# Kernel tuning notes

Measured on AMD Instinct MI355X. Metric: run time of the kernel, lower is better.

Reference implementation:

```python
import jax, jax.numpy as jnp
import numpy as np

D_MODEL = 768
N_HEADS = 12
D_HEAD = D_MODEL // N_HEADS


def setup_inputs() -> dict:
    key = jax.random.key(0)
    ks = jax.random.split(key, 6)
    B, T = 2, 4096
    x = jax.random.normal(ks[0], (B, T, D_MODEL), dtype=jnp.float32)
    mask = jnp.ones((B, T), dtype=jnp.int32)
    # torch nn.Linear: weight [out, in], bias [out]
    s_in = 1.0 / np.sqrt(D_MODEL)
    w_qkv = jax.random.uniform(ks[1], (3 * D_MODEL, D_MODEL), jnp.float32, -s_in, s_in)
    b_qkv = jax.random.uniform(ks[2], (3 * D_MODEL,), jnp.float32, -s_in, s_in)
    w_out = jax.random.uniform(ks[3], (D_MODEL, D_MODEL), jnp.float32, -s_in, s_in)
    b_out = jax.random.uniform(ks[4], (D_MODEL,), jnp.float32, -s_in, s_in)
    return {"x": x, "w_qkv": w_qkv, "b_qkv": b_qkv, "w_out": w_out, "b_out": b_out, "mask": mask}


def reference(x, w_qkv, b_qkv, w_out, b_out, mask):
    B, T, C = x.shape
    # fused QKV projection: [B,T,3C]
    qkv = x @ w_qkv.T + b_qkv
    qkv = qkv.reshape(B, T, 3, N_HEADS, D_HEAD)
    qkv = jnp.transpose(qkv, (2, 0, 3, 1, 4))  # [3,B,H,T,Dh]
    q, k, v = qkv[0], qkv[1], qkv[2]
    scale = jnp.float32(np.sqrt(D_HEAD))
    scores = jnp.einsum('bhqd,bhkd->bhqk', q, k) / scale  # [B,H,T,T]
    scores = jnp.where(mask[:, None, None, :] == 0, jnp.float32(-1e9), scores)
    weights = jax.nn.softmax(scores, axis=-1)  # dropout p=0 (eval-mode reference)
    out = jnp.einsum('bhqk,bhkd->bhqd', weights, v)  # [B,H,T,Dh]
    out = jnp.transpose(out, (0, 2, 1, 3)).reshape(B, T, C)
    return out @ w_out.T + b_out
```

## Files before the change

kernel.cpp:

```cpp
#include <hip/hip_runtime.h>
#include <hip/hip_bf16.h>
#include <cstdint>
#include <cstddef>

#define D_MODEL 768
#define N_HEADS 12
#define T_SEQ   4096
#define B_BATCH 2
#define BT      (B_BATCH * T_SEQ)

typedef __attribute__((ext_vector_type(8))) short bf16x8;
typedef __attribute__((ext_vector_type(4))) float f32x4;

__device__ __forceinline__ short fbf(float f) {
  __hip_bfloat16 h = __float2bfloat16(f);
  return __builtin_bit_cast(short, h);
}

__device__ __forceinline__ void gl_lds16(const void* g, void* l) {
  __builtin_amdgcn_global_load_lds(
      (const __attribute__((address_space(1))) void*)g,
      (__attribute__((address_space(3))) void*)l, 16, 0, 0);
}

__global__ __launch_bounds__(256) void cast_bf16(const float* __restrict__ in,
                                                 short* __restrict__ out, int n8) {
  int i = blockIdx.x * 256 + threadIdx.x;
  if (i >= n8) return;
  const float4* p = (const float4*)in + (size_t)i * 2;
  float4 v0 = p[0], v1 = p[1];
  bf16x8 o;
  o[0] = fbf(v0.x); o[1] = fbf(v0.y); o[2] = fbf(v0.z); o[3] = fbf(v0.w);
  o[4] = fbf(v1.x); o[5] = fbf(v1.y); o[6] = fbf(v1.z); o[7] = fbf(v1.w);
  *(bf16x8*)(out + (size_t)i * 8) = o;
}

__global__ __launch_bounds__(256) void mask_prep(const int* __restrict__ mask,
                                                 short* __restrict__ maskpb) {
  int t = blockIdx.x * 256 + threadIdx.x;
  int blk = t >> 6, j = t & 63;
  int pj = (((j >> 4) & 1) << 5) | (((j >> 2) & 3) << 3) | (((j >> 5) & 1) << 2) | (j & 3);
  maskpb[blk * 64 + pj] = mask[t] ? (short)0x3F80 : (short)0;
}

template<int EPI>
__global__ __launch_bounds__(256) void gemm_bt(
    const short* __restrict__ A, const short* __restrict__ Bm,
    const float* __restrict__ bias, int K, int N,
    short* __restrict__ Qb, short* __restrict__ Kb, short* __restrict__ Vt,
    const int* __restrict__ maskp, float* __restrict__ Cout)
{
  __shared__ __align__(16) short As[128 * 64];
  __shared__ __align__(16) short Bs[128 * 64];

  const int t = threadIdx.x;
  const int lane = t & 63, wave = t >> 6;
  const int a = lane & 15, g = lane >> 4;
  const int wr = wave >> 1, wc = wave & 1;
  const int bm = blockIdx.x * 128, bn = blockIdx.y * 128;

  f32x4 acc[4][4];
  #pragma unroll
  for (int i = 0; i < 4; ++i)
    #pragma unroll
    for (int j = 0; j < 4; ++j) acc[i][j] = f32x4{0.f, 0.f, 0.f, 0.f};

  const int nkt = K >> 6;
  for (int kt = 0; kt < nkt; ++kt) {
    const int k0 = kt << 6;
    __syncthreads();
    #pragma unroll
    for (int it = 0; it < 4; ++it) {
      int cid = it * 256 + t;
      int row = cid >> 3, c16 = cid & 7;
      int sc = c16 ^ (row & 7);
      gl_lds16(A  + (size_t)(bm + row) * K + k0 + sc * 8, (char*)As + (it * 256 + wave * 64) * 16);
      gl_lds16(Bm + (size_t)(bn + row) * K + k0 + sc * 8, (char*)Bs + (it * 256 + wave * 64) * 16);
    }
    __syncthreads();
    #pragma unroll
    for (int c = 0; c < 2; ++c) {
      bf16x8 af[4], bfr[4];
      #pragma unroll
      for (int mi = 0; mi < 4; ++mi) {
        int row = wr * 64 + mi * 16 + a;
        af[mi] = *(const bf16x8*)((const char*)As + row * 128 + ((c * 64 + g * 16) ^ ((row & 7) << 4)));
      }
      #pragma unroll
      for (int ni = 0; ni < 4; ++ni) {
        int row = wc * 64 + ni * 16 + a;
        bfr[ni] = *(const bf16x8*)((const char*)Bs + row * 128 + ((c * 64 + g * 16) ^ ((row & 7) << 4)));
      }
      #pragma unroll
      for (int mi = 0; mi < 4; ++mi)
        #pragma unroll
        for (int ni = 0; ni < 4; ++ni)
          acc[mi][ni] = __builtin_amdgcn_mfma_f32_16x16x32_bf16(af[mi], bfr[ni], acc[mi][ni], 0, 0, 0);
    }
  }

  if (EPI == 1) {
    #pragma unroll
    for (int mi = 0; mi < 4; ++mi) {
      int rowb = bm + wr * 64 + mi * 16 + g * 4;
      #pragma unroll
      for (int ni = 0; ni < 4; ++ni) {
        int col = bn + wc * 64 + ni * 16 + a;
        float bv = bias[col];
        #pragma unroll
        for (int r = 0; r < 4; ++r)
          Cout[(size_t)(rowb + r) * N + col] = acc[mi][ni][r] + bv;
      }
    }
  } else {
    const float QSCALE = 0.125f * 1.44269504088896f;
    const int sec = bn / D_MODEL;
    #pragma unroll
    for (int ni = 0; ni < 4; ++ni) {
      int n = bn + wc * 64 + ni * 16 + a;
      int wcol = n - sec * D_MODEL;
      int h = wcol >> 6, d = wcol & 63;
      float bv = bias[n];
      #pragma unroll
      for (int mi = 0; mi < 4; ++mi) {
        #pragma unroll
        for (int r = 0; r < 4; ++r) {
          int mrow = bm + wr * 64 + mi * 16 + g * 4 + r;
          int bb = mrow >> 12, tt = mrow & 4095;
          float val = acc[mi][ni][r] + bv;
          size_t bhoff = (size_t)(bb * N_HEADS + h);
          if (sec == 0)       Qb[(bhoff * T_SEQ + tt) * 64 + d] = fbf(val * QSCALE);
          else if (sec == 1)  Kb[(bhoff * T_SEQ + tt) * 64 + d] = fbf(val);
          else {
            val *= (float)maskp[(size_t)bb * T_SEQ + tt];
            int t6 = tt & 63;
            int ttp = (tt & ~63) | (((t6 >> 4) & 1) << 5) | (((t6 >> 2) & 3) << 3)
                    | (((t6 >> 5) & 1) << 2) | (t6 & 3);
            Vt[(bhoff * 64 + d) * T_SEQ + ttp] = fbf(val);
          }
        }
      }
    }
  }
}

__global__ __launch_bounds__(256, 3) void attn(
    const short* __restrict__ Qb, const short* __restrict__ Kb, const short* __restrict__ Vt,
    const short* __restrict__ maskpb, short* __restrict__ Ao)
{
  __shared__ __align__(16) short Kt[2][64 * 64];
  __shared__ __align__(16) short Vs[2][64 * 64];

  const int t = threadIdx.x;
  const int lane = t & 63, wave = t >> 6;
  const int a = lane & 15, g = lane >> 4;

  const int flat = blockIdx.x;
  const int xcd = flat & 7, slot = flat >> 3;
  const int logical = xcd * 96 + slot;
  const int bh = logical >> 5;
  const int qblk = logical & 31;

  const int b = bh / N_HEADS, h = bh - b * N_HEADS;
  const size_t headoff = (size_t)bh * T_SEQ * 64;
  const int q0 = qblk * 128 + wave * 32;

  const int srow0 = t >> 3, sc0 = (t & 7) ^ (srow0 & 7);
  const int srow1 = (256 + t) >> 3, sc1 = (t & 7) ^ (srow1 & 7);
  const short* Kh = Kb + headoff;
  const short* Vh = Vt + headoff;
  const short* mh = maskpb + (size_t)b * T_SEQ;

  bf16x8 qf[2][2];
  #pragma unroll
  for (int qg = 0; qg < 2; ++qg) {
    const short* qrow = Qb + headoff + (size_t)(q0 + qg * 16 + a) * 64;
    qf[qg][0] = *(const bf16x8*)(qrow + g * 8);
    qf[qg][1] = *(const bf16x8*)(qrow + 32 + g * 8);
  }

  int foff[2][4];
  #pragma unroll
  for (int c = 0; c < 2; ++c)
    #pragma unroll
    for (int ni = 0; ni < 4; ++ni) {
      int row = ni * 16 + a;
      foff[c][ni] = row * 128 + ((c * 64 + g * 16) ^ ((row & 7) << 4));
    }

  f32x4 o[2][4];
  f32x4 ladd[2];
  #pragma unroll
  for (int qg = 0; qg < 2; ++qg) {
    ladd[qg] = f32x4{0.f, 0.f, 0.f, 0.f};
    #pragma unroll
    for (int i = 0; i < 4; ++i) o[qg][i] = f32x4{0.f, 0.f, 0.f, 0.f};
  }

#define STAGE(buf, kb)                                                                   \
  do {                                                                                   \
    gl_lds16(Kh + (size_t)((kb) + srow0) * 64 + sc0 * 8, (char*)Kt[buf] + (wave * 64) * 16);          \
    gl_lds16(Vh + (size_t)srow0 * T_SEQ + (kb) + sc0 * 8, (char*)Vs[buf] + (wave * 64) * 16);         \
    gl_lds16(Kh + (size_t)((kb) + srow1) * 64 + sc1 * 8, (char*)Kt[buf] + (256 + wave * 64) * 16);    \
    gl_lds16(Vh + (size_t)srow1 * T_SEQ + (kb) + sc1 * 8, (char*)Vs[buf] + (256 + wave * 64) * 16);   \
  } while (0)

  STAGE(0, 0);
  __syncthreads();

  const int NT = T_SEQ / 64;
  int cur = 0;
  for (int kt = 0; kt < NT; ++kt) {
    const int kb = kt * 64;
    if (kt + 1 < NT) STAGE(cur ^ 1, kb + 64);

    f32x4 st[2][4];
    #pragma unroll
    for (int qg = 0; qg < 2; ++qg)
      #pragma unroll
      for (int ni = 0; ni < 4; ++ni) st[qg][ni] = f32x4{0.f,0.f,0.f,0.f};

    __builtin_amdgcn_s_setprio(1);
    #pragma unroll
    for (int c = 0; c < 2; ++c) {
      #pragma unroll
      for (int ni = 0; ni < 4; ++ni) {
        bf16x8 kf = *(const bf16x8*)((const char*)Kt[cur] + foff[c][ni]);
        st[0][ni] = __builtin_amdgcn_mfma_f32_16x16x32_bf16(kf, qf[0][c], st[0][ni], 0, 0, 0);
        st[1][ni] = __builtin_amdgcn_mfma_f32_16x16x32_bf16(kf, qf[1][c], st[1][ni], 0, 0, 0);
      }
    }
    __builtin_amdgcn_s_setprio(0);

    bf16x8 pa[2][2];
    #pragma unroll
    for (int qg = 0; qg < 2; ++qg)
      #pragma unroll
      for (int ni = 0; ni < 4; ++ni) {
        const int c = ni & 1, jb = (ni >> 1) * 4;
        #pragma unroll
        for (int r = 0; r < 4; ++r)
          pa[qg][c][jb + r] = fbf(__builtin_amdgcn_exp2f(st[qg][ni][r]));
      }

    __builtin_amdgcn_s_setprio(1);
    #pragma unroll
    for (int c = 0; c < 2; ++c) {
      bf16x8 mbf = *(const bf16x8*)(mh + kb + c * 32 + g * 8);
      ladd[0] = __builtin_amdgcn_mfma_f32_16x16x32_bf16(pa[0][c], mbf, ladd[0], 0, 0, 0);
      ladd[1] = __builtin_amdgcn_mfma_f32_16x16x32_bf16(pa[1][c], mbf, ladd[1], 0, 0, 0);
      #pragma unroll
      for (int di = 0; di < 4; ++di) {
        bf16x8 vf = *(const bf16x8*)((const char*)Vs[cur] + foff[c][di]);
        o[0][di] = __builtin_amdgcn_mfma_f32_16x16x32_bf16(pa[0][c], vf, o[0][di], 0, 0, 0);
        o[1][di] = __builtin_amdgcn_mfma_f32_16x16x32_bf16(pa[1][c], vf, o[1][di], 0, 0, 0);
      }
    }
    __builtin_amdgcn_s_setprio(0);

    __syncthreads();
    cur ^= 1;
  }
#undef STAGE

  #pragma unroll
  for (int qg = 0; qg < 2; ++qg) {
    float linv[4];
    #pragma unroll
    for (int r = 0; r < 4; ++r) linv[r] = 1.f / ladd[qg][r];
    #pragma unroll
    for (int di = 0; di < 4; ++di)
      #pragma unroll
      for (int r = 0; r < 4; ++r) {
        int rowg = b * T_SEQ + q0 + qg * 16 + g * 4 + r;
        Ao[(size_t)rowg * D_MODEL + h * 64 + di * 16 + a] = fbf(o[qg][di][r] * linv[r]);
      }
  }
}

extern "C" void kernel_launch(void* const* d_in, const int* in_sizes, int n_in,
                              void* d_out, int out_size, void* d_ws, size_t ws_size,
                              hipStream_t stream) {
  const float* x     = (const float*)d_in[0];
  const float* w_qkv = (const float*)d_in[1];
  const float* b_qkv = (const float*)d_in[2];
  const float* w_out = (const float*)d_in[3];
  const float* b_out = (const float*)d_in[4];
  const int*   mask  = (const int*)d_in[5];
  float* out = (float*)d_out;

  char* w = (char*)d_ws;
  short* xb     = (short*)w; w += (size_t)BT * D_MODEL * 2;
  short* wqkvb  = (short*)w; w += (size_t)3 * D_MODEL * D_MODEL * 2;
  short* woutb  = (short*)w; w += (size_t)D_MODEL * D_MODEL * 2;
  short* Qb     = (short*)w; w += (size_t)BT * D_MODEL * 2;
  short* Kb     = (short*)w; w += (size_t)BT * D_MODEL * 2;
  short* Vt     = (short*)w; w += (size_t)BT * D_MODEL * 2;
  short* Ao     = (short*)w; w += (size_t)BT * D_MODEL * 2;
  short* maskpb = (short*)w; w += (size_t)BT * 2;

  {
    int n8 = BT * D_MODEL / 8;
    cast_bf16<<<n8 / 256, 256, 0, stream>>>(x, xb, n8);
  }
  {
    int n8 = 3 * D_MODEL * D_MODEL / 8;
    cast_bf16<<<n8 / 256, 256, 0, stream>>>(w_qkv, wqkvb, n8);
  }
  {
    int n8 = D_MODEL * D_MODEL / 8;
    cast_bf16<<<n8 / 256, 256, 0, stream>>>(w_out, woutb, n8);
  }
  mask_prep<<<BT / 256, 256, 0, stream>>>(mask, maskpb);

  gemm_bt<0><<<dim3(BT / 128, 3 * D_MODEL / 128), 256, 0, stream>>>(
      xb, wqkvb, b_qkv, D_MODEL, 3 * D_MODEL, Qb, Kb, Vt, mask, nullptr);

  attn<<<768, 256, 0, stream>>>(Qb, Kb, Vt, maskpb, Ao);

  gemm_bt<1><<<dim3(BT / 128, D_MODEL / 128), 256, 0, stream>>>(
      Ao, woutb, b_out, D_MODEL, D_MODEL, nullptr, nullptr, nullptr, nullptr, out);
}
```

Before: 268.6 us.

## Triple-buffer attention K/V, fold mask into K/V, coalesce V-transpose stores

The attention loop moves from double to triple buffering of K/V tiles in LDS. It uses an explicit vmcnt wait and a single barrier per iteration, so loads for tile kt+2 overlap compute on tile kt. The per-tile mask load in the row-sum MFMA is removed: masked keys get K and V zeroed in the QKV epilogue, the row sum uses a constant ones vector, and the count of masked keys is subtracted from the denominator. The V epilogue now stages the transposed, permuted tile through LDS so global stores are coalesced. LDS use per block rises, and the denominator trick depends on masked scores being exactly zero.

```diff
diff --git a/kernel.cpp b/kernel.cpp
--- a/kernel.cpp
+++ b/kernel.cpp
@@ -35,12 +35,18 @@
   *(bf16x8*)(out + (size_t)i * 8) = o;
 }
 
-__global__ __launch_bounds__(256) void mask_prep(const int* __restrict__ mask,
-                                                 short* __restrict__ maskpb) {
-  int t = blockIdx.x * 256 + threadIdx.x;
-  int blk = t >> 6, j = t & 63;
-  int pj = (((j >> 4) & 1) << 5) | (((j >> 2) & 3) << 3) | (((j >> 5) & 1) << 2) | (j & 3);
-  maskpb[blk * 64 + pj] = mask[t] ? (short)0x3F80 : (short)0;
+__global__ __launch_bounds__(256) void mask_count(const int* __restrict__ mask,
+                                                  float* __restrict__ nm) {
+  __shared__ int red[256];
+  int s = 0;
+  for (int i = threadIdx.x; i < T_SEQ; i += 256) s += mask[blockIdx.x * T_SEQ + i];
+  red[threadIdx.x] = s;
+  __syncthreads();
+  for (int off = 128; off > 0; off >>= 1) {
+    if (threadIdx.x < off) red[threadIdx.x] += red[threadIdx.x + off];
+    __syncthreads();
+  }
+  if (threadIdx.x == 0) nm[blockIdx.x] = (float)(T_SEQ - red[0]);
 }
 
 template<int EPI>
@@ -50,8 +56,11 @@
     short* __restrict__ Qb, short* __restrict__ Kb, short* __restrict__ Vt,
     const int* __restrict__ maskp, float* __restrict__ Cout)
 {
-  __shared__ __align__(16) short As[128 * 64];
-  __shared__ __align__(16) short Bs[128 * 64];
+  __shared__ __align__(16) short smem[128 * 132];
+  short* As = smem;
+  short* Bs = smem + 128 * 64;
+  typedef short CtRow[132];
+  CtRow* Ct = (CtRow*)smem;
 
   const int t = threadIdx.x;
   const int lane = t & 63, wave = t >> 6;
@@ -115,41 +124,66 @@
   } else {
     const float QSCALE = 0.125f * 1.44269504088896f;
     const int sec = bn / D_MODEL;
-    #pragma unroll
-    for (int ni = 0; ni < 4; ++ni) {
-      int n = bn + wc * 64 + ni * 16 + a;
-      int wcol = n - sec * D_MODEL;
-      int h = wcol >> 6, d = wcol & 63;
-      float bv = bias[n];
-      #pragma unroll
-      for (int mi = 0; mi < 4; ++mi) {
-        #pragma unroll
-        for (int r = 0; r < 4; ++r) {
-          int mrow = bm + wr * 64 + mi * 16 + g * 4 + r;
-          int bb = mrow >> 12, tt = mrow & 4095;
-          float val = acc[mi][ni][r] + bv;
-          size_t bhoff = (size_t)(bb * N_HEADS + h);
-          if (sec == 0)       Qb[(bhoff * T_SEQ + tt) * 64 + d] = fbf(val * QSCALE);
-          else if (sec == 1)  Kb[(bhoff * T_SEQ + tt) * 64 + d] = fbf(val);
-          else {
-            val *= (float)maskp[(size_t)bb * T_SEQ + tt];
-            int t6 = tt & 63;
-            int ttp = (tt & ~63) | (((t6 >> 4) & 1) << 5) | (((t6 >> 2) & 3) << 3)
-                    | (((t6 >> 5) & 1) << 2) | (t6 & 3);
-            Vt[(bhoff * 64 + d) * T_SEQ + ttp] = fbf(val);
+    const int bb = bm >> 12, tt0 = bm & 4095;
+    if (sec < 2) {
+      #pragma unroll
+      for (int ni = 0; ni < 4; ++ni) {
+        int n = bn + wc * 64 + ni * 16 + a;
+        int wcol = n - sec * D_MODEL;
+        int h = wcol >> 6, d = wcol & 63;
+        float bv = bias[n];
+        size_t bhoff = (size_t)(bb * N_HEADS + h);
+        #pragma unroll
+        for (int mi = 0; mi < 4; ++mi) {
+          #pragma unroll
+          for (int r = 0; r < 4; ++r) {
+            int tt = tt0 + wr * 64 + mi * 16 + g * 4 + r;
+            float val = acc[mi][ni][r] + bv;
+            if (sec == 0) Qb[(bhoff * T_SEQ + tt) * 64 + d] = fbf(val * QSCALE);
+            else          Kb[(bhoff * T_SEQ + tt) * 64 + d] =
+                              fbf(val * (float)maskp[(size_t)bb * T_SEQ + tt]);
           }
         }
       }
+    } else {
+      __syncthreads();
+      #pragma unroll
+      for (int ni = 0; ni < 4; ++ni) {
+        int col_t = wc * 64 + ni * 16 + a;
+        float bv = bias[bn + col_t];
+        #pragma unroll
+        for (int mi = 0; mi < 4; ++mi) {
+          #pragma unroll
+          for (int r = 0; r < 4; ++r) {
+            int rowin = wr * 64 + mi * 16 + g * 4 + r;
+            int tt = tt0 + rowin;
+            float val = (acc[mi][ni][r] + bv) * (float)maskp[(size_t)bb * T_SEQ + tt];
+            int t6 = rowin & 63;
+            int rowp = (rowin & 64) | (((t6 >> 4) & 1) << 5) | (((t6 >> 2) & 3) << 3)
+                     | (((t6 >> 5) & 1) << 2) | (t6 & 3);
+            Ct[col_t][rowp] = fbf(val);
+          }
+        }
+      }
+      __syncthreads();
+      const int wb = bn - 2 * D_MODEL;
+      #pragma unroll
+      for (int it = 0; it < 32; ++it) {
+        int col = wave * 32 + it;
+        int wcol = wb + col;
+        int h = wcol >> 6, d = wcol & 63;
+        size_t base = ((size_t)(bb * N_HEADS + h) * 64 + d) * T_SEQ + tt0;
+        *(short2*)(Vt + base + 2 * lane) = *(const short2*)&Ct[col][2 * lane];
+      }
     }
   }
 }
 
 __global__ __launch_bounds__(256, 3) void attn(
     const short* __restrict__ Qb, const short* __restrict__ Kb, const short* __restrict__ Vt,
-    const short* __restrict__ maskpb, short* __restrict__ Ao)
+    const float* __restrict__ nmasked, short* __restrict__ Ao)
 {
-  __shared__ __align__(16) short Kt[2][64 * 64];
-  __shared__ __align__(16) short Vs[2][64 * 64];
+  __shared__ __align__(16) short KV[3][2][64 * 64];
 
   const int t = threadIdx.x;
   const int lane = t & 63, wave = t >> 6;
@@ -169,7 +203,7 @@
   const int srow1 = (256 + t) >> 3, sc1 = (t & 7) ^ (srow1 & 7);
   const short* Kh = Kb + headoff;
   const short* Vh = Vt + headoff;
-  const short* mh = maskpb + (size_t)b * T_SEQ;
+  const float nm = nmasked[b];
 
   bf16x8 qf[2][2];
   #pragma unroll
@@ -179,6 +213,10 @@
     qf[qg][1] = *(const bf16x8*)(qrow + 32 + g * 8);
   }
 
+  bf16x8 ones;
+  #pragma unroll
+  for (int i = 0; i < 8; ++i) ones[i] = (short)0x3F80;
+
   int foff[2][4];
   #pragma unroll
   for (int c = 0; c < 2; ++c)
@@ -197,22 +235,27 @@
     for (int i = 0; i < 4; ++i) o[qg][i] = f32x4{0.f, 0.f, 0.f, 0.f};
   }
 
-#define STAGE(buf, kb)                                                                   \
-  do {                                                                                   \
-    gl_lds16(Kh + (size_t)((kb) + srow0) * 64 + sc0 * 8, (char*)Kt[buf] + (wave * 64) * 16);          \
-    gl_lds16(Vh + (size_t)srow0 * T_SEQ + (kb) + sc0 * 8, (char*)Vs[buf] + (wave * 64) * 16);         \
-    gl_lds16(Kh + (size_t)((kb) + srow1) * 64 + sc1 * 8, (char*)Kt[buf] + (256 + wave * 64) * 16);    \
-    gl_lds16(Vh + (size_t)srow1 * T_SEQ + (kb) + sc1 * 8, (char*)Vs[buf] + (256 + wave * 64) * 16);   \
+#define STAGE(buf, kb)                                                                        \
+  do {                                                                                        \
+    gl_lds16(Kh + (size_t)((kb) + srow0) * 64 + sc0 * 8,  (char*)KV[buf][0] + (wave * 64) * 16);       \
+    gl_lds16(Vh + (size_t)srow0 * T_SEQ + (kb) + sc0 * 8, (char*)KV[buf][1] + (wave * 64) * 16);       \
+    gl_lds16(Kh + (size_t)((kb) + srow1) * 64 + sc1 * 8,  (char*)KV[buf][0] + (256 + wave * 64) * 16); \
+    gl_lds16(Vh + (size_t)srow1 * T_SEQ + (kb) + sc1 * 8, (char*)KV[buf][1] + (256 + wave * 64) * 16); \
   } while (0)
 
   STAGE(0, 0);
-  __syncthreads();
+  STAGE(1, 64);
 
   const int NT = T_SEQ / 64;
-  int cur = 0;
+  int cur = 0, nx2 = 2;
   for (int kt = 0; kt < NT; ++kt) {
-    const int kb = kt * 64;
-    if (kt + 1 < NT) STAGE(cur ^ 1, kb + 64);
+    if (kt < NT - 1) asm volatile("s_waitcnt vmcnt(4)" ::: "memory");
+    else             asm volatile("s_waitcnt vmcnt(0)" ::: "memory");
+    __builtin_amdgcn_s_barrier();
+    if (kt + 2 < NT) STAGE(nx2, (kt + 2) * 64);
+
+    const char* Ktc = (const char*)KV[cur][0];
+    const char* Vsc = (const char*)KV[cur][1];
 
     f32x4 st[2][4];
     #pragma unroll
@@ -225,7 +268,7 @@
     for (int c = 0; c < 2; ++c) {
       #pragma unroll
       for (int ni = 0; ni < 4; ++ni) {
-        bf16x8 kf = *(const bf16x8*)((const char*)Kt[cur] + foff[c][ni]);
+        bf16x8 kf = *(const bf16x8*)(Ktc + foff[c][ni]);
         st[0][ni] = __builtin_amdgcn_mfma_f32_16x16x32_bf16(kf, qf[0][c], st[0][ni], 0, 0, 0);
         st[1][ni] = __builtin_amdgcn_mfma_f32_16x16x32_bf16(kf, qf[1][c], st[1][ni], 0, 0, 0);
       }
@@ -246,20 +289,19 @@
     __builtin_amdgcn_s_setprio(1);
     #pragma unroll
     for (int c = 0; c < 2; ++c) {
-      bf16x8 mbf = *(const bf16x8*)(mh + kb + c * 32 + g * 8);
-      ladd[0] = __builtin_amdgcn_mfma_f32_16x16x32_bf16(pa[0][c], mbf, ladd[0], 0, 0, 0);
-      ladd[1] = __builtin_amdgcn_mfma_f32_16x16x32_bf16(pa[1][c], mbf, ladd[1], 0, 0, 0);
+      ladd[0] = __builtin_amdgcn_mfma_f32_16x16x32_bf16(pa[0][c], ones, ladd[0], 0, 0, 0);
+      ladd[1] = __builtin_amdgcn_mfma_f32_16x16x32_bf16(pa[1][c], ones, ladd[1], 0, 0, 0);
       #pragma unroll
       for (int di = 0; di < 4; ++di) {
-        bf16x8 vf = *(const bf16x8*)((const char*)Vs[cur] + foff[c][di]);
+        bf16x8 vf = *(const bf16x8*)(Vsc + foff[c][di]);
         o[0][di] = __builtin_amdgcn_mfma_f32_16x16x32_bf16(pa[0][c], vf, o[0][di], 0, 0, 0);
         o[1][di] = __builtin_amdgcn_mfma_f32_16x16x32_bf16(pa[1][c], vf, o[1][di], 0, 0, 0);
       }
     }
     __builtin_amdgcn_s_setprio(0);
 
-    __syncthreads();
-    cur ^= 1;
+    cur = cur + 1; if (cur == 3) cur = 0;
+    nx2 = nx2 + 1; if (nx2 == 3) nx2 = 0;
   }
 #undef STAGE
 
@@ -267,7 +309,7 @@
   for (int qg = 0; qg < 2; ++qg) {
     float linv[4];
     #pragma unroll
-    for (int r = 0; r < 4; ++r) linv[r] = 1.f / ladd[qg][r];
+    for (int r = 0; r < 4; ++r) linv[r] = 1.f / (ladd[qg][r] - nm);
     #pragma unroll
     for (int di = 0; di < 4; ++di)
       #pragma unroll
@@ -290,14 +332,14 @@
   float* out = (float*)d_out;
 
   char* w = (char*)d_ws;
-  short* xb     = (short*)w; w += (size_t)BT * D_MODEL * 2;
-  short* wqkvb  = (short*)w; w += (size_t)3 * D_MODEL * D_MODEL * 2;
-  short* woutb  = (short*)w; w += (size_t)D_MODEL * D_MODEL * 2;
-  short* Qb     = (short*)w; w += (size_t)BT * D_MODEL * 2;
-  short* Kb     = (short*)w; w += (size_t)BT * D_MODEL * 2;
-  short* Vt     = (short*)w; w += (size_t)BT * D_MODEL * 2;
-  short* Ao     = (short*)w; w += (size_t)BT * D_MODEL * 2;
-  short* maskpb = (short*)w; w += (size_t)BT * 2;
+  short* xb    = (short*)w; w += (size_t)BT * D_MODEL * 2;
+  short* wqkvb = (short*)w; w += (size_t)3 * D_MODEL * D_MODEL * 2;
+  short* woutb = (short*)w; w += (size_t)D_MODEL * D_MODEL * 2;
+  short* Qb    = (short*)w; w += (size_t)BT * D_MODEL * 2;
+  short* Kb    = (short*)w; w += (size_t)BT * D_MODEL * 2;
+  short* Vt    = (short*)w; w += (size_t)BT * D_MODEL * 2;
+  short* Ao    = (short*)w; w += (size_t)BT * D_MODEL * 2;
+  float* nm    = (float*)w; w += 2 * sizeof(float);
 
   {
     int n8 = BT * D_MODEL / 8;
@@ -311,12 +353,12 @@
     int n8 = D_MODEL * D_MODEL / 8;
     cast_bf16<<<n8 / 256, 256, 0, stream>>>(w_out, woutb, n8);
   }
-  mask_prep<<<BT / 256, 256, 0, stream>>>(mask, maskpb);
+  mask_count<<<2, 256, 0, stream>>>(mask, nm);
 
   gemm_bt<0><<<dim3(BT / 128, 3 * D_MODEL / 128), 256, 0, stream>>>(
       xb, wqkvb, b_qkv, D_MODEL, 3 * D_MODEL, Qb, Kb, Vt, mask, nullptr);
 
-  attn<<<768, 256, 0, stream>>>(Qb, Kb, Vt, maskpb, Ao);
+  attn<<<768, 256, 0, stream>>>(Qb, Kb, Vt, nm, Ao);
 
   gemm_bt<1><<<dim3(BT / 128, D_MODEL / 128), 256, 0, stream>>>(
       Ao, woutb, b_out, D_MODEL, D_MODEL, nullptr, nullptr, nullptr, nullptr, out);
```

New measurement: 255.8 us. -4.8%, faster.
